# Kernel optimization log

Measured on AMD Instinct MI355X. Metric: run time of the kernel, lower is better.

Reference implementation:

```python
import jax, jax.numpy as jnp
import numpy as np

B, H, T, K, V = 2, 8, 2048, 128, 128


def setup_inputs() -> dict:
    key = jax.random.key(0)
    k1, k2, k3, k4, k5 = jax.random.split(key, 5)
    return {
        "q": jax.random.normal(k1, (B, H, T, K), dtype=jnp.float32),
        "k": jax.random.normal(k2, (B, H, T, K), dtype=jnp.float32),
        "v": jax.random.normal(k3, (B, H, T, V), dtype=jnp.float32),
        "i_gate": jax.random.normal(k4, (B, H, T), dtype=jnp.float32),
        "f_gate": jax.random.normal(k5, (B, H, T), dtype=jnp.float32),
    }


def reference(q, k, v, i_gate, f_gate):
    # Stabilized parallel mLSTM (same math as the chunked Triton kernel,
    # expressed in natural-log base instead of base-2).
    Bq, Hq, Tq, Kd = q.shape
    scale = Kd ** -0.5
    logf = jax.nn.log_sigmoid(f_gate)                      # [B,H,T]
    fc = jnp.cumsum(logf, axis=-1)                         # cumulative forget logits
    # log decay matrix: logD[t,s] = i[s] + (fc[t] - fc[s]) for s <= t
    logD = fc[..., :, None] - fc[..., None, :] + i_gate[..., None, :]  # [B,H,T,T]
    mask = jnp.tril(jnp.ones((Tq, Tq), dtype=bool))
    logD_masked = jnp.where(mask, logD, -jnp.inf)
    m = jnp.max(logD_masked, axis=-1)                      # row-wise stabilizer [B,H,T]
    D = jnp.where(mask, jnp.exp(logD - m[..., None]), 0.0) # stabilized decay matrix
    S = jnp.einsum("bhtk,bhsk->bhts", q, k) * scale * D    # gated scores
    norm = jnp.maximum(jnp.abs(jnp.sum(S, axis=-1)), jnp.exp(-m))  # [B,H,T]
    h = jnp.einsum("bhts,bhsv->bhtv", S, v) / norm[..., None]
    return h
```

## Files before the change

kernel.cpp:

```cpp
#include <hip/hip_runtime.h>

#define T_SEQ 2048
#define DHEAD 128
#define NBH 16
#define SCALE 0.08838834764831845f

typedef unsigned short u16;
typedef u16 u16x4 __attribute__((ext_vector_type(4)));
typedef u16 u16x8 __attribute__((ext_vector_type(8)));
typedef __bf16 bf16x8 __attribute__((ext_vector_type(8)));
typedef float f32x16 __attribute__((ext_vector_type(16)));

__device__ __forceinline__ u16 f2bfu(float x) {
  union { float f; unsigned u; } c; c.f = x;
  unsigned u = c.u;
  u = u + 0x7FFFu + ((u >> 16) & 1u);
  return (u16)(u >> 16);
}

__device__ __forceinline__ bf16x8 ldsFrag(const u16* p) {
  u16x8 t = *(const u16x8*)p;
  return __builtin_bit_cast(bf16x8, t);
}

__device__ __forceinline__ void gld_lds16(const void* g, void* l) {
  __builtin_amdgcn_global_load_lds(
      (__attribute__((address_space(1))) const unsigned int*)g,
      (__attribute__((address_space(3))) unsigned int*)l, 16, 0, 0);
}

__global__ __launch_bounds__(256) void gate_scan_kernel(
    const float* __restrict__ ig, const float* __restrict__ fg,
    float* __restrict__ a_out, float* __restrict__ c_out,
    float* __restrict__ fc_out)
{
  const int bh  = blockIdx.x;
  const int tid = threadIdx.x;
  const int base = bh * T_SEQ + tid * 8;
  __shared__ float sbuf[256];

  float lf[8];
  float run = 0.f;
#pragma unroll
  for (int j = 0; j < 8; ++j) {
    float x  = fg[base + j];
    float ls = fminf(x, 0.f) - log1pf(expf(-fabsf(x)));
    run += ls; lf[j] = run;
  }
  sbuf[tid] = run; __syncthreads();
  for (int off = 1; off < 256; off <<= 1) {
    float t = (tid >= off) ? sbuf[tid - off] : 0.f;
    __syncthreads();
    sbuf[tid] += t;
    __syncthreads();
  }
  const float excl = (tid > 0) ? sbuf[tid - 1] : 0.f;
  __syncthreads();

  float fc[8], cm[8];
  float runm = -INFINITY;
#pragma unroll
  for (int j = 0; j < 8; ++j) {
    fc[j] = excl + lf[j];
    fc_out[base + j] = fc[j];
    float av = ig[base + j] - fc[j];
    a_out[base + j] = av;
    runm = fmaxf(runm, av);
    cm[j] = runm;
  }
  sbuf[tid] = runm; __syncthreads();
  for (int off = 1; off < 256; off <<= 1) {
    float t = (tid >= off) ? sbuf[tid - off] : -INFINITY;
    __syncthreads();
    sbuf[tid] = fmaxf(sbuf[tid], t);
    __syncthreads();
  }
  const float exclm = (tid > 0) ? sbuf[tid - 1] : -INFINITY;
#pragma unroll
  for (int j = 0; j < 8; ++j) {
    c_out[base + j] = fmaxf(exclm, cm[j]);
  }
}

__global__ __launch_bounds__(256) void cvt_k_kernel(
    const float* __restrict__ src, u16* __restrict__ dst)
{
  const int i = (blockIdx.x * 256 + threadIdx.x) * 4;
  const float4 x = *(const float4*)(src + i);
  u16x4 p; p[0] = f2bfu(x.x); p[1] = f2bfu(x.y); p[2] = f2bfu(x.z); p[3] = f2bfu(x.w);
  *(u16x4*)(dst + i) = p;
}

__global__ __launch_bounds__(256) void cvt_vt_kernel(
    const float* __restrict__ v, u16* __restrict__ vt)
{
  const int bh = blockIdx.y, kt = blockIdx.x, tid = threadIdx.x;
  __shared__ __align__(16) u16 L[128 * 72];
  const int n0 = (tid & 31) * 4, k0 = (tid >> 5) * 8;
  const float* vp = v + ((size_t)bh * T_SEQ + kt * 64 + k0) * DHEAD + n0;
  u16 tv[4][8];
#pragma unroll
  for (int rr = 0; rr < 8; ++rr) {
    const float4 x = *(const float4*)(vp + rr * DHEAD);
    tv[0][rr] = f2bfu(x.x); tv[1][rr] = f2bfu(x.y);
    tv[2][rr] = f2bfu(x.z); tv[3][rr] = f2bfu(x.w);
  }
#pragma unroll
  for (int j = 0; j < 4; ++j) {
    u16x8 p;
#pragma unroll
    for (int rr = 0; rr < 8; ++rr) p[rr] = tv[j][rr];
    *(u16x8*)(&L[(n0 + j) * 72 + k0]) = p;
  }
  __syncthreads();
  const int row = tid >> 1, s0 = (tid & 1) * 32;
  u16* op = vt + ((size_t)bh * DHEAD + row) * T_SEQ + kt * 64 + s0;
#pragma unroll
  for (int i = 0; i < 4; ++i)
    *(u16x8*)(op + i * 8) = *(const u16x8*)(&L[row * 72 + s0 + i * 8]);
}

template <bool FAST>
__global__ __launch_bounds__(512, 2) void mlstm_fwd_kernel(
    const float* __restrict__ qg, const float* __restrict__ kg,
    const float* __restrict__ vg,
    const u16* __restrict__ kbf, const u16* __restrict__ vtbf,
    const float* __restrict__ ag, const float* __restrict__ cg,
    const float* __restrict__ fcg, float* __restrict__ out)
{
  const int bx = (int)blockIdx.x;
  const int bh = bx & 15, p = bx >> 4;
  const int tid = (int)threadIdx.x;
  const int w8 = tid >> 6, lane = tid & 63;
  const int hh = lane >> 5, l32 = lane & 31;

  const int qsel  = w8 >> 2;
  const int half  = (w8 >> 1) & 1;
  const int strip = w8 & 1;
  const int qt    = qsel ? p : (31 - p);
  const int nST   = 32 - p;
  const int diagST = qsel ? p : (31 - p);
  const int qrow0 = qt * 64 + strip * 32;

  __shared__ __align__(16) unsigned char SM[81920];
  u16* Plw = (u16*)(SM + 65536 + w8 * 2048);

  const size_t hoff = (size_t)bh * T_SEQ * DHEAD;
  const int goff = bh * T_SEQ;

  bf16x8 qf[8];
  {
    const float* qp = qg + hoff + (size_t)(qrow0 + l32) * DHEAD + hh * 8;
#pragma unroll
    for (int ks_ = 0; ks_ < 8; ++ks_) {
      const float4 x0 = *(const float4*)(qp + ks_ * 16);
      const float4 x1 = *(const float4*)(qp + ks_ * 16 + 4);
      u16x8 t;
      t[0] = f2bfu(x0.x); t[1] = f2bfu(x0.y); t[2] = f2bfu(x0.z); t[3] = f2bfu(x0.w);
      t[4] = f2bfu(x1.x); t[5] = f2bfu(x1.y); t[6] = f2bfu(x1.z); t[7] = f2bfu(x1.w);
      qf[ks_] = __builtin_bit_cast(bf16x8, t);
    }
  }
  const float cmax = cg[goff + qt * 64 + 63];

  f32x16 oa[4];
#pragma unroll
  for (int nt = 0; nt < 4; ++nt)
#pragma unroll
    for (int r = 0; r < 16; ++r) oa[nt][r] = 0.f;
  float rs[16];
#pragma unroll
  for (int r = 0; r < 16; ++r) rs[r] = 0.f;

  float kr[2][8], vr[2][8];

  auto stage_issue = [&](int st, int b) {
    if (FAST) {
      const u16* ks = kbf + ((size_t)goff + st * 64) * DHEAD;
      const u16* vs = vtbf + (size_t)bh * DHEAD * T_SEQ + st * 64;
#pragma unroll
      for (int j = 0; j < 2; ++j) {
        const int B = (w8 * 2 + j) * 64 + lane;
        {
          const int key = B >> 4;
          const int db = (B & 15) ^ (key & 7);
          gld_lds16(ks + (size_t)key * DHEAD + db * 8,
                    (u16*)(SM + b * 32768) + (w8 * 2 + j) * 512);
        }
        {
          const int n = B >> 3;
          const int kb = (B & 7) ^ (n & 7);
          gld_lds16(vs + (size_t)n * T_SEQ + kb * 8,
                    (u16*)(SM + b * 32768 + 16384) + (w8 * 2 + j) * 512);
        }
      }
    } else {
      const float* kp = kg + hoff + (size_t)(st * 64) * DHEAD;
      const float* vp = vg + hoff + (size_t)(st * 64) * DHEAD;
#pragma unroll
      for (int j = 0; j < 2; ++j) {
        const int B = (w8 * 2 + j) * 64 + lane;
        const int key = B >> 4;
        const int db = (B & 15) ^ (key & 7);
        const float4 x0 = *(const float4*)(kp + (size_t)key * DHEAD + db * 8);
        const float4 x1 = *(const float4*)(kp + (size_t)key * DHEAD + db * 8 + 4);
        kr[j][0] = x0.x; kr[j][1] = x0.y; kr[j][2] = x0.z; kr[j][3] = x0.w;
        kr[j][4] = x1.x; kr[j][5] = x1.y; kr[j][6] = x1.z; kr[j][7] = x1.w;
        const int n = B >> 3;
        const int kb = (B & 7) ^ (n & 7);
#pragma unroll
        for (int rr = 0; rr < 8; ++rr)
          vr[j][rr] = vp[(size_t)(kb * 8 + rr) * DHEAD + n];
      }
    }
  };
  auto stage_commit = [&](int b) {
    if (!FAST) {
#pragma unroll
      for (int j = 0; j < 2; ++j) {
        u16x8 pk, pv;
#pragma unroll
        for (int rr = 0; rr < 8; ++rr) { pk[rr] = f2bfu(kr[j][rr]); pv[rr] = f2bfu(vr[j][rr]); }
        *(u16x8*)((u16*)(SM + b * 32768) + (w8 * 2 + j) * 512 + lane * 8) = pk;
        *(u16x8*)((u16*)(SM + b * 32768 + 16384) + (w8 * 2 + j) * 512 + lane * 8) = pv;
      }
    }
  };

  stage_issue(0, 0);
  stage_commit(0);
  __syncthreads();

  const int plc = (lane >> 3) & 3, pl7 = lane & 7;

  for (int st = 0; st < nST; ++st) {
    const int b = st & 1;
    if (st + 1 < nST) stage_issue(st + 1, b ^ 1);

    const bool act = (qsel == 0) || (st <= p);
    if (act) {
      const int keyl = half * 32 + l32;
      const int keyg = st * 64 + keyl;
      const float av = ag[goff + keyg];
      const u16* Kb_ = (const u16*)(SM + b * 32768);
      const u16* Vb_ = (const u16*)(SM + b * 32768 + 16384);

      f32x16 s;
#pragma unroll
      for (int r = 0; r < 16; ++r) s[r] = 0.f;
#pragma unroll
      for (int ks_ = 0; ks_ < 8; ++ks_) {
        const int db = 2 * ks_ + hh;
        const bf16x8 bk = ldsFrag(Kb_ + keyl * 128 + ((db ^ (keyl & 7)) * 8));
        s = __builtin_amdgcn_mfma_f32_32x32x16_bf16(qf[ks_], bk, s, 0, 0, 0);
      }
      const float es = SCALE * __expf(av - cmax);
      const bool diag = (st == diagST);
#pragma unroll
      for (int reg = 0; reg < 16; ++reg) {
        const int rowl = (reg & 3) + 8 * (reg >> 2) + 4 * hh;
        float pv = s[reg] * es;
        if (diag && (keyg > qrow0 + rowl)) pv = 0.f;
        rs[reg] += pv;
        Plw[rowl * 32 + ((plc ^ (rowl & 3)) * 8) + pl7] = f2bfu(pv);
      }
#pragma unroll
      for (int k2 = 0; k2 < 2; ++k2) {
        const int cb = 2 * k2 + hh;
        const bf16x8 pa = ldsFrag(Plw + l32 * 32 + ((cb ^ (l32 & 3)) * 8));
        const int kb = half * 4 + 2 * k2 + hh;
#pragma unroll
        for (int nt = 0; nt < 4; ++nt) {
          const int n = nt * 32 + l32;
          const bf16x8 bv = ldsFrag(Vb_ + n * 64 + ((kb ^ (n & 7)) * 8));
          oa[nt] = __builtin_amdgcn_mfma_f32_32x32x16_bf16(pa, bv, oa[nt], 0, 0, 0);
        }
      }
    }
    if (st + 1 < nST) stage_commit(b ^ 1);
    __syncthreads();
  }

  float* osh = (float*)SM;
  float* rsh = (float*)(SM + 65536);
  const int combo = qsel * 2 + strip;

#pragma unroll
  for (int reg = 0; reg < 16; ++reg) {
    float x = rs[reg];
#pragma unroll
    for (int off = 1; off < 32; off <<= 1) x += __shfl_xor(x, off, 64);
    rs[reg] = x;
  }

  if (half == 1) {
#pragma unroll
    for (int nt = 0; nt < 4; ++nt)
#pragma unroll
      for (int reg = 0; reg < 16; ++reg) {
        const int rowl = (reg & 3) + 8 * (reg >> 2) + 4 * hh;
        osh[combo * 4096 + rowl * 128 + nt * 32 + l32] = oa[nt][reg];
      }
    if (l32 == 0) {
#pragma unroll
      for (int reg = 0; reg < 16; ++reg) {
        const int rowl = (reg & 3) + 8 * (reg >> 2) + 4 * hh;
        rsh[combo * 32 + rowl] = rs[reg];
      }
    }
  }
  __syncthreads();
  if (half == 0) {
    float inv[16];
#pragma unroll
    for (int reg = 0; reg < 16; ++reg) {
      const int rowl = (reg & 3) + 8 * (reg >> 2) + 4 * hh;
      const float rtot = rs[reg] + rsh[combo * 32 + rowl];
      const float fcv = fcg[goff + qrow0 + rowl];
      inv[reg] = 1.f / fmaxf(fabsf(rtot), __expf(-(cmax + fcv)));
    }
    float* op = out + hoff;
#pragma unroll
    for (int nt = 0; nt < 4; ++nt)
#pragma unroll
      for (int reg = 0; reg < 16; ++reg) {
        const int rowl = (reg & 3) + 8 * (reg >> 2) + 4 * hh;
        const float ov = oa[nt][reg] + osh[combo * 4096 + rowl * 128 + nt * 32 + l32];
        op[(size_t)(qrow0 + rowl) * DHEAD + nt * 32 + l32] = ov * inv[reg];
      }
  }
}

extern "C" void kernel_launch(void* const* d_in, const int* in_sizes, int n_in,
                              void* d_out, int out_size, void* d_ws, size_t ws_size,
                              hipStream_t stream) {
  const float* q  = (const float*)d_in[0];
  const float* k  = (const float*)d_in[1];
  const float* v  = (const float*)d_in[2];
  const float* ig = (const float*)d_in[3];
  const float* fg = (const float*)d_in[4];

  const size_t gate_bytes = (size_t)3 * NBH * T_SEQ * sizeof(float);
  const size_t kv_elems   = (size_t)NBH * T_SEQ * DHEAD;
  const bool fast = ws_size >= gate_bytes + 2 * kv_elems * sizeof(u16);

  float* a_ws  = (float*)d_ws;
  float* c_ws  = a_ws + NBH * T_SEQ;
  float* fc_ws = c_ws + NBH * T_SEQ;
  u16* kbf  = (u16*)((char*)d_ws + gate_bytes);
  u16* vtbf = kbf + kv_elems;

  gate_scan_kernel<<<dim3(NBH), dim3(256), 0, stream>>>(ig, fg, a_ws, c_ws, fc_ws);
  if (fast) {
    cvt_k_kernel<<<dim3((unsigned)(kv_elems / 1024)), dim3(256), 0, stream>>>(k, kbf);
    cvt_vt_kernel<<<dim3(T_SEQ / 64, NBH), dim3(256), 0, stream>>>(v, vtbf);
    mlstm_fwd_kernel<true><<<dim3(256), dim3(512), 0, stream>>>(
        q, k, v, kbf, vtbf, a_ws, c_ws, fc_ws, (float*)d_out);
  } else {
    mlstm_fwd_kernel<false><<<dim3(256), dim3(512), 0, stream>>>(
        q, k, v, kbf, vtbf, a_ws, c_ws, fc_ws, (float*)d_out);
  }
}
```

Before: 150.7 us.

## Fold key gate scale into bf16 K and keep P in registers via transposed MFMA

```diff
diff --git a/kernel.cpp b/kernel.cpp
--- a/kernel.cpp
+++ b/kernel.cpp
@@ -6,8 +6,10 @@
 #define SCALE 0.08838834764831845f
 
 typedef unsigned short u16;
+typedef unsigned int u32;
 typedef u16 u16x4 __attribute__((ext_vector_type(4)));
 typedef u16 u16x8 __attribute__((ext_vector_type(8)));
+typedef u32 u32x4 __attribute__((ext_vector_type(4)));
 typedef __bf16 bf16x8 __attribute__((ext_vector_type(8)));
 typedef float f32x16 __attribute__((ext_vector_type(16)));
 
@@ -16,6 +18,10 @@
   unsigned u = c.u;
   u = u + 0x7FFFu + ((u >> 16) & 1u);
   return (u16)(u >> 16);
+}
+
+__device__ __forceinline__ u32 packbf2(float lo, float hi) {
+  return (u32)f2bfu(lo) | ((u32)f2bfu(hi) << 16);
 }
 
 __device__ __forceinline__ bf16x8 ldsFrag(const u16* p) {
@@ -83,11 +89,16 @@
 }
 
 __global__ __launch_bounds__(256) void cvt_k_kernel(
-    const float* __restrict__ src, u16* __restrict__ dst)
+    const float* __restrict__ src, const float* __restrict__ ag,
+    const float* __restrict__ cg, u16* __restrict__ dst)
 {
   const int i = (blockIdx.x * 256 + threadIdx.x) * 4;
+  const int bhs = i >> 7;
+  const float sc = __expf(ag[bhs] - cg[bhs | 63]);
   const float4 x = *(const float4*)(src + i);
-  u16x4 p; p[0] = f2bfu(x.x); p[1] = f2bfu(x.y); p[2] = f2bfu(x.z); p[3] = f2bfu(x.w);
+  u16x4 p;
+  p[0] = f2bfu(x.x * sc); p[1] = f2bfu(x.y * sc);
+  p[2] = f2bfu(x.z * sc); p[3] = f2bfu(x.w * sc);
   *(u16x4*)(dst + i) = p;
 }
 
@@ -121,7 +132,7 @@
 }
 
 template <bool FAST>
-__global__ __launch_bounds__(512, 2) void mlstm_fwd_kernel(
+__global__ __launch_bounds__(512, 1) void mlstm_fwd_kernel(
     const float* __restrict__ qg, const float* __restrict__ kg,
     const float* __restrict__ vg,
     const u16* __restrict__ kbf, const u16* __restrict__ vtbf,
@@ -139,26 +150,26 @@
   const int strip = w8 & 1;
   const int qt    = qsel ? p : (31 - p);
   const int nST   = 32 - p;
-  const int diagST = qsel ? p : (31 - p);
   const int qrow0 = qt * 64 + strip * 32;
-
-  __shared__ __align__(16) unsigned char SM[81920];
-  u16* Plw = (u16*)(SM + 65536 + w8 * 2048);
+  const int qrowg = qrow0 + l32;
+
+  __shared__ __align__(16) unsigned char SM[65536];
+  __shared__ float rsh[128];
 
   const size_t hoff = (size_t)bh * T_SEQ * DHEAD;
   const int goff = bh * T_SEQ;
 
   bf16x8 qf[8];
   {
-    const float* qp = qg + hoff + (size_t)(qrow0 + l32) * DHEAD + hh * 8;
-#pragma unroll
-    for (int ks_ = 0; ks_ < 8; ++ks_) {
-      const float4 x0 = *(const float4*)(qp + ks_ * 16);
-      const float4 x1 = *(const float4*)(qp + ks_ * 16 + 4);
+    const float* qp = qg + hoff + (size_t)qrowg * DHEAD + hh * 8;
+#pragma unroll
+    for (int ks = 0; ks < 8; ++ks) {
+      const float4 x0 = *(const float4*)(qp + ks * 16);
+      const float4 x1 = *(const float4*)(qp + ks * 16 + 4);
       u16x8 t;
       t[0] = f2bfu(x0.x); t[1] = f2bfu(x0.y); t[2] = f2bfu(x0.z); t[3] = f2bfu(x0.w);
       t[4] = f2bfu(x1.x); t[5] = f2bfu(x1.y); t[6] = f2bfu(x1.z); t[7] = f2bfu(x1.w);
-      qf[ks_] = __builtin_bit_cast(bf16x8, t);
+      qf[ks] = __builtin_bit_cast(bf16x8, t);
     }
   }
   const float cmax = cg[goff + qt * 64 + 63];
@@ -168,9 +179,7 @@
   for (int nt = 0; nt < 4; ++nt)
 #pragma unroll
     for (int r = 0; r < 16; ++r) oa[nt][r] = 0.f;
-  float rs[16];
-#pragma unroll
-  for (int r = 0; r < 16; ++r) rs[r] = 0.f;
+  float rsacc = 0.f;
 
   float kr[2][8], vr[2][8];
 
@@ -195,6 +204,7 @@
         }
       }
     } else {
+      const float ct = cg[goff + st * 64 + 63];
       const float* kp = kg + hoff + (size_t)(st * 64) * DHEAD;
       const float* vp = vg + hoff + (size_t)(st * 64) * DHEAD;
 #pragma unroll
@@ -202,10 +212,11 @@
         const int B = (w8 * 2 + j) * 64 + lane;
         const int key = B >> 4;
         const int db = (B & 15) ^ (key & 7);
+        const float sc = __expf(ag[goff + st * 64 + key] - ct);
         const float4 x0 = *(const float4*)(kp + (size_t)key * DHEAD + db * 8);
         const float4 x1 = *(const float4*)(kp + (size_t)key * DHEAD + db * 8 + 4);
-        kr[j][0] = x0.x; kr[j][1] = x0.y; kr[j][2] = x0.z; kr[j][3] = x0.w;
-        kr[j][4] = x1.x; kr[j][5] = x1.y; kr[j][6] = x1.z; kr[j][7] = x1.w;
+        kr[j][0] = x0.x * sc; kr[j][1] = x0.y * sc; kr[j][2] = x0.z * sc; kr[j][3] = x0.w * sc;
+        kr[j][4] = x1.x * sc; kr[j][5] = x1.y * sc; kr[j][6] = x1.z * sc; kr[j][7] = x1.w * sc;
         const int n = B >> 3;
         const int kb = (B & 7) ^ (n & 7);
 #pragma unroll
@@ -218,11 +229,12 @@
     if (!FAST) {
 #pragma unroll
       for (int j = 0; j < 2; ++j) {
-        u16x8 pk, pv;
-#pragma unroll
-        for (int rr = 0; rr < 8; ++rr) { pk[rr] = f2bfu(kr[j][rr]); pv[rr] = f2bfu(vr[j][rr]); }
-        *(u16x8*)((u16*)(SM + b * 32768) + (w8 * 2 + j) * 512 + lane * 8) = pk;
-        *(u16x8*)((u16*)(SM + b * 32768 + 16384) + (w8 * 2 + j) * 512 + lane * 8) = pv;
+        const int B = (w8 * 2 + j) * 64 + lane;
+        u16x8 pk, pw;
+#pragma unroll
+        for (int rr = 0; rr < 8; ++rr) { pk[rr] = f2bfu(kr[j][rr]); pw[rr] = f2bfu(vr[j][rr]); }
+        *(u16x8*)((u16*)(SM + b * 32768) + B * 8) = pk;
+        *(u16x8*)((u16*)(SM + b * 32768 + 16384) + B * 8) = pw;
       }
     }
   };
@@ -231,49 +243,70 @@
   stage_commit(0);
   __syncthreads();
 
-  const int plc = (lane >> 3) & 3, pl7 = lane & 7;
-
   for (int st = 0; st < nST; ++st) {
     const int b = st & 1;
     if (st + 1 < nST) stage_issue(st + 1, b ^ 1);
 
-    const bool act = (qsel == 0) || (st <= p);
+    const bool act = (qsel == 0) || (st <= qt);
     if (act) {
-      const int keyl = half * 32 + l32;
-      const int keyg = st * 64 + keyl;
-      const float av = ag[goff + keyg];
       const u16* Kb_ = (const u16*)(SM + b * 32768);
       const u16* Vb_ = (const u16*)(SM + b * 32768 + 16384);
-
-      f32x16 s;
-#pragma unroll
-      for (int r = 0; r < 16; ++r) s[r] = 0.f;
-#pragma unroll
-      for (int ks_ = 0; ks_ < 8; ++ks_) {
-        const int db = 2 * ks_ + hh;
-        const bf16x8 bk = ldsFrag(Kb_ + keyl * 128 + ((db ^ (keyl & 7)) * 8));
-        s = __builtin_amdgcn_mfma_f32_32x32x16_bf16(qf[ks_], bk, s, 0, 0, 0);
-      }
-      const float es = SCALE * __expf(av - cmax);
-      const bool diag = (st == diagST);
+      const int keyl = half * 32 + l32;
+
+      f32x16 s0, s1;
+#pragma unroll
+      for (int r = 0; r < 16; ++r) { s0[r] = 0.f; s1[r] = 0.f; }
+#pragma unroll
+      for (int k2 = 0; k2 < 4; ++k2) {
+        {
+          const int db = 2 * (2 * k2) + hh;
+          const bf16x8 kf = ldsFrag(Kb_ + keyl * 128 + ((db ^ (keyl & 7)) * 8));
+          s0 = __builtin_amdgcn_mfma_f32_32x32x16_bf16(kf, qf[2 * k2], s0, 0, 0, 0);
+        }
+        {
+          const int db = 2 * (2 * k2 + 1) + hh;
+          const bf16x8 kf = ldsFrag(Kb_ + keyl * 128 + ((db ^ (keyl & 7)) * 8));
+          s1 = __builtin_amdgcn_mfma_f32_32x32x16_bf16(kf, qf[2 * k2 + 1], s1, 0, 0, 0);
+        }
+      }
+      const float etile = SCALE * __expf(cg[goff + st * 64 + 63] - cmax);
+      const bool diag = (st == qt);
+
+      float pv[16];
+      float r0 = 0.f, r1 = 0.f, r2 = 0.f, r3 = 0.f;
 #pragma unroll
       for (int reg = 0; reg < 16; ++reg) {
-        const int rowl = (reg & 3) + 8 * (reg >> 2) + 4 * hh;
-        float pv = s[reg] * es;
-        if (diag && (keyg > qrow0 + rowl)) pv = 0.f;
-        rs[reg] += pv;
-        Plw[rowl * 32 + ((plc ^ (rowl & 3)) * 8) + pl7] = f2bfu(pv);
+        float x = (s0[reg] + s1[reg]) * etile;
+        if (diag) {
+          const int rowl = (reg & 3) + 8 * (reg >> 2) + 4 * hh;
+          if (st * 64 + half * 32 + rowl > qrowg) x = 0.f;
+        }
+        pv[reg] = x;
+        if ((reg & 3) == 0) r0 += x; else if ((reg & 3) == 1) r1 += x;
+        else if ((reg & 3) == 2) r2 += x; else r3 += x;
+      }
+      rsacc += (r0 + r1) + (r2 + r3);
+
+      u32 d8[8];
+#pragma unroll
+      for (int q = 0; q < 4; ++q) {
+        d8[2 * q]     = packbf2(pv[4 * q],     pv[4 * q + 1]);
+        d8[2 * q + 1] = packbf2(pv[4 * q + 2], pv[4 * q + 3]);
       }
 #pragma unroll
       for (int k2 = 0; k2 < 2; ++k2) {
-        const int cb = 2 * k2 + hh;
-        const bf16x8 pa = ldsFrag(Plw + l32 * 32 + ((cb ^ (l32 & 3)) * 8));
-        const int kb = half * 4 + 2 * k2 + hh;
+        const int qo = 2 * k2 + (hh ^ 1), qn = 2 * k2 + hh;
+        const u32 e0 = __shfl_xor(d8[2 * qo], 32, 64);
+        const u32 e1 = __shfl_xor(d8[2 * qo + 1], 32, 64);
+        const u32x4 fw = hh ? (u32x4){e0, e1, d8[2 * qn], d8[2 * qn + 1]}
+                            : (u32x4){d8[2 * qn], d8[2 * qn + 1], e0, e1};
+        const bf16x8 pfrag = __builtin_bit_cast(bf16x8, fw);
+        const int kb = half * 4 + k2 * 2 + hh;
 #pragma unroll
         for (int nt = 0; nt < 4; ++nt) {
           const int n = nt * 32 + l32;
-          const bf16x8 bv = ldsFrag(Vb_ + n * 64 + ((kb ^ (n & 7)) * 8));
-          oa[nt] = __builtin_amdgcn_mfma_f32_32x32x16_bf16(pa, bv, oa[nt], 0, 0, 0);
+          const bf16x8 vf = ldsFrag(Vb_ + n * 64 + ((kb ^ (n & 7)) * 8));
+          oa[nt] = __builtin_amdgcn_mfma_f32_32x32x16_bf16(vf, pfrag, oa[nt], 0, 0, 0);
         }
       }
     }
@@ -281,52 +314,37 @@
     __syncthreads();
   }
 
+  rsacc += __shfl_xor(rsacc, 32, 64);
+  const int combo = qsel * 2 + strip;
   float* osh = (float*)SM;
-  float* rsh = (float*)(SM + 65536);
-  const int combo = qsel * 2 + strip;
-
-#pragma unroll
-  for (int reg = 0; reg < 16; ++reg) {
-    float x = rs[reg];
-#pragma unroll
-    for (int off = 1; off < 32; off <<= 1) x += __shfl_xor(x, off, 64);
-    rs[reg] = x;
-  }
 
   if (half == 1) {
 #pragma unroll
     for (int nt = 0; nt < 4; ++nt)
 #pragma unroll
       for (int reg = 0; reg < 16; ++reg) {
-        const int rowl = (reg & 3) + 8 * (reg >> 2) + 4 * hh;
-        osh[combo * 4096 + rowl * 128 + nt * 32 + l32] = oa[nt][reg];
-      }
-    if (l32 == 0) {
-#pragma unroll
-      for (int reg = 0; reg < 16; ++reg) {
-        const int rowl = (reg & 3) + 8 * (reg >> 2) + 4 * hh;
-        rsh[combo * 32 + rowl] = rs[reg];
-      }
-    }
+        const int rown = (reg & 3) + 8 * (reg >> 2) + 4 * hh;
+        osh[combo * 4096 + (nt * 32 + rown) * 32 + l32] = oa[nt][reg];
+      }
+    if (hh == 0) rsh[combo * 32 + l32] = rsacc;
   }
   __syncthreads();
   if (half == 0) {
-    float inv[16];
-#pragma unroll
-    for (int reg = 0; reg < 16; ++reg) {
-      const int rowl = (reg & 3) + 8 * (reg >> 2) + 4 * hh;
-      const float rtot = rs[reg] + rsh[combo * 32 + rowl];
-      const float fcv = fcg[goff + qrow0 + rowl];
-      inv[reg] = 1.f / fmaxf(fabsf(rtot), __expf(-(cmax + fcv)));
-    }
-    float* op = out + hoff;
+    const float rstot = rsacc + rsh[combo * 32 + l32];
+    const float nf = __expf(-(cmax + fcg[goff + qrowg]));
+    const float inv = 1.f / fmaxf(fabsf(rstot), nf);
+    float* op = out + hoff + (size_t)qrowg * DHEAD;
 #pragma unroll
     for (int nt = 0; nt < 4; ++nt)
 #pragma unroll
-      for (int reg = 0; reg < 16; ++reg) {
-        const int rowl = (reg & 3) + 8 * (reg >> 2) + 4 * hh;
-        const float ov = oa[nt][reg] + osh[combo * 4096 + rowl * 128 + nt * 32 + l32];
-        op[(size_t)(qrow0 + rowl) * DHEAD + nt * 32 + l32] = ov * inv[reg];
+      for (int q = 0; q < 4; ++q) {
+        float4 ov;
+        const int base = combo * 4096 + (nt * 32 + 8 * q + 4 * hh) * 32 + l32;
+        ov.x = (oa[nt][4 * q]     + osh[base])      * inv;
+        ov.y = (oa[nt][4 * q + 1] + osh[base + 32]) * inv;
+        ov.z = (oa[nt][4 * q + 2] + osh[base + 64]) * inv;
+        ov.w = (oa[nt][4 * q + 3] + osh[base + 96]) * inv;
+        *(float4*)(op + nt * 32 + 8 * q + 4 * hh) = ov;
       }
   }
 }
@@ -352,7 +370,8 @@
 
   gate_scan_kernel<<<dim3(NBH), dim3(256), 0, stream>>>(ig, fg, a_ws, c_ws, fc_ws);
   if (fast) {
-    cvt_k_kernel<<<dim3((unsigned)(kv_elems / 1024)), dim3(256), 0, stream>>>(k, kbf);
+    cvt_k_kernel<<<dim3((unsigned)(kv_elems / 1024)), dim3(256), 0, stream>>>(
+        k, a_ws, c_ws, kbf);
     cvt_vt_kernel<<<dim3(T_SEQ / 64, NBH), dim3(256), 0, stream>>>(v, vtbf);
     mlstm_fwd_kernel<true><<<dim3(256), dim3(512), 0, stream>>>(
         q, k, v, kbf, vtbf, a_ws, c_ws, fc_ws, (float*)d_out);
```

New measurement: 165.9 us. 10.1% more time.
